# Performance work log

Hardware: AMD Instinct MI355X
Metric: run time of the kernel (lower is better)

Reference implementation:

```python
import jax, jax.numpy as jnp
import numpy as np

B, L, H, E = 8, 1024, 8, 64
S, D = 1024, 64


def fp(x):
    # power-norm with p=2: norm(x) * x^2 / norm(x^2)
    norm = jnp.sqrt(jnp.sum(x * x, axis=-1, keepdims=True))
    px = x * x  # x^p, p=2
    pnorm = jnp.sqrt(jnp.sum(px * px, axis=-1, keepdims=True))
    return norm * px / pnorm


def phi_p(x):
    return fp(jax.nn.relu(x))


def setup_inputs() -> dict:
    key = jax.random.key(0)
    kq, kk, kv = jax.random.split(key, 3)
    queries = jax.random.normal(kq, (B, L, H, E), dtype=jnp.float32)
    keys = jax.random.normal(kk, (B, S, H, E), dtype=jnp.float32)
    values = jax.random.normal(kv, (B, S, H, D), dtype=jnp.float32)
    # all-False mask: masked_fill(-inf) + fp() would NaN otherwise (see notes)
    attn_mask = jnp.zeros((B, 1, L, S), dtype=bool)
    return {"queries": queries, "keys": keys, "values": values, "attn_mask": attn_mask}


def reference(queries, keys, values, attn_mask):
    qt = phi_p(queries)              # [B,L,H,E]
    kt = phi_p(keys)                 # [B,S,H,E]
    scores = jnp.einsum('blhe,bshe->bhls', qt, kt)  # [B,H,L,S]
    scores = jnp.where(attn_mask, -jnp.inf, scores)  # mask_flag=True path
    # NB: original computes scale = 1/sqrt(E) but never applies it.
    A = jax.nn.softmax(fp(scores), axis=-1)  # dropout is identity at eval
    V = jnp.einsum('bhls,bshd->blhd', A, values)  # [B,L,H,D]
    return V
```

## Files before the change

### kernel.cpp

```cpp
#include <hip/hip_runtime.h>
#include <hip/hip_bf16.h>


#define B_ 8
#define L_ 1024
#define H_ 8
#define E_ 64
#define S_ 1024
#define D_ 64
#define BH_ 64

typedef _Float16 f16_t;
typedef _Float16 f16x8 __attribute__((ext_vector_type(8)));
typedef _Float16 f16x4v __attribute__((ext_vector_type(4)));
typedef float f32x4 __attribute__((ext_vector_type(4)));
typedef unsigned u32x4 __attribute__((ext_vector_type(4)));

#define MFMA16F(a, b, c) __builtin_amdgcn_mfma_f32_16x16x32_f16(a, b, c, 0, 0, 0)
#define GLDS16(g, l)                                                        \
  __builtin_amdgcn_global_load_lds(                                         \
      (const __attribute__((address_space(1))) void*)(g),                   \
      (__attribute__((address_space(3))) void*)(l), 16, 0, 0)

#if __has_builtin(__builtin_amdgcn_exp2f)
#define EXP2(x) __builtin_amdgcn_exp2f(x)
#else
#define EXP2(x) exp2f(x)
#endif

static __device__ __forceinline__ unsigned pkh(float a, float b) {
  return __builtin_bit_cast(unsigned, __builtin_amdgcn_cvt_pkrtz(a, b));
}

static __device__ __forceinline__ void pl32_swap(unsigned& x, unsigned& y) {
#if __has_builtin(__builtin_amdgcn_permlane32_swap)
  auto r = __builtin_amdgcn_permlane32_swap(x, y, false, false);
  x = r[0];
  y = r[1];
#else
  unsigned xs = __shfl_xor((int)x, 32, 64), ys = __shfl_xor((int)y, 32, 64);
  bool hi = (threadIdx.x & 32) != 0;
  unsigned nx = hi ? ys : x;
  unsigned ny = hi ? y : xs;
  x = nx;
  y = ny;
#endif
}

static __device__ __forceinline__ void pl16_swap(unsigned& x, unsigned& y) {
#if __has_builtin(__builtin_amdgcn_permlane16_swap)
  auto r = __builtin_amdgcn_permlane16_swap(x, y, false, false);
  x = r[0];
  y = r[1];
#else
  unsigned xs = __shfl_xor((int)x, 16, 64), ys = __shfl_xor((int)y, 16, 64);
  bool odd = (threadIdx.x & 16) != 0;
  unsigned nx = odd ? ys : x;
  unsigned ny = odd ? y : xs;
  x = nx;
  y = ny;
#endif
}

__global__ __launch_bounds__(256) void prep_kernel(
    const float* __restrict__ q, const float* __restrict__ k,
    const float* __restrict__ v, f16_t* __restrict__ qf,
    f16_t* __restrict__ kf, f16_t* __restrict__ vt) {
  __shared__ float tile[32][68];
  int bid = blockIdx.x;
  if (bid < 8192) {
    int row = bid * 16 + (threadIdx.x >> 4);
    int p = threadIdx.x & 15;
    const float* src;
    f16_t* dst;
    int r = row;
    if (r < B_ * L_ * H_) { src = q; dst = qf; }
    else { r -= B_ * L_ * H_; src = k; dst = kf; }
    int b = r >> 13;
    int l = (r >> 3) & 1023;
    int h = r & 7;
    float4 x = ((const float4*)(src + (size_t)r * 64))[p];
    float s0 = fmaxf(x.x, 0.f) * fmaxf(x.x, 0.f);
    float s1 = fmaxf(x.y, 0.f) * fmaxf(x.y, 0.f);
    float s2 = fmaxf(x.z, 0.f) * fmaxf(x.z, 0.f);
    float s3 = fmaxf(x.w, 0.f) * fmaxf(x.w, 0.f);
    float sum2 = (s0 + s1) + (s2 + s3);
    float sum4 = fmaf(s0, s0, s1 * s1) + fmaf(s2, s2, s3 * s3);
#pragma unroll
    for (int off = 1; off < 16; off <<= 1) {
      sum2 += __shfl_xor(sum2, off, 64);
      sum4 += __shfl_xor(sum4, off, 64);
    }
    float sc = (sum4 > 0.f) ? sqrtf(sum2 / sum4) : 0.f;
    f16x4v o = {(f16_t)(sc * s0), (f16_t)(sc * s1), (f16_t)(sc * s2),
                (f16_t)(sc * s3)};
    int c = p >> 1, e = (p & 1) * 4;
    int col = (((c ^ (l & 7)) << 3) | e);
    *(f16x4v*)(dst + ((size_t)(b * H_ + h) * 1024 + l) * 64 + col) = o;
  } else {
    int vb = bid - 8192;
    int bh = vb >> 5;
    int st = vb & 31;
    int b = bh >> 3, h = bh & 7;
    int t = threadIdx.x;
    int sl = t >> 3, dp = t & 7;
    const float* src =
        v + (((size_t)(b * S_ + st * 32 + sl) * H_ + h) * D_) + dp * 8;
    float4 f0 = ((const float4*)src)[0];
    float4 f1 = ((const float4*)src)[1];
    *(float4*)&tile[sl][dp * 8] = f0;
    *(float4*)&tile[sl][dp * 8 + 4] = f1;
    __syncthreads();
    int d = t >> 2, sc = t & 3;
    f16_t tmp[8];
#pragma unroll
    for (int j = 0; j < 8; ++j) tmp[j] = (f16_t)tile[sc * 8 + j][d];
    f16_t* dst = vt + (((size_t)bh * 32 + st) * 64 + d) * 32 + sc * 8;
    *(uint4*)dst = *(const uint4*)tmp;
  }
}

__global__ __launch_bounds__(256, 2) void attn_kernel(
    const f16_t* __restrict__ qf, const f16_t* __restrict__ kf,
    const f16_t* __restrict__ vt, float* __restrict__ out) {
  __shared__ __align__(16) f16_t k_t[2][2048];
  __shared__ __align__(16) f16_t v_t[2][2048];

  int bh = blockIdx.x & 63;
  int qb = blockIdx.x >> 6;
  int b = bh >> 3, h = bh & 7;
  int tid = threadIdx.x;
  int wave = tid >> 6, lane = tid & 63;
  int g = lane >> 4, n = lane & 15;

  const f16_t* qf_b = qf + ((size_t)bh * L_ + qb * 128) * 64;
  const f16_t* kf_b = kf + (size_t)bh * S_ * 64;
  const f16_t* vt_b = vt + (size_t)bh * 32 * 2048;

  int arow = wave * 32 + n;
  int qoff0 = arow * 64 + ((g ^ (n & 7)) << 3);
  int qoff1 = qoff0 + 16 * 64;
  f16x8 qa0_0 = *(const f16x8*)(qf_b + qoff0);
  f16x8 qa1_0 = *(const f16x8*)(qf_b + (qoff0 ^ 32));
  f16x8 qa0_1 = *(const f16x8*)(qf_b + qoff1);
  f16x8 qa1_1 = *(const f16x8*)(qf_b + (qoff1 ^ 32));

  int koff = n * 64 + ((g ^ (n & 7)) << 3);
  int lds_o = tid * 8;

  const f32x4 fzero = {0.f, 0.f, 0.f, 0.f};
  f32x4 acc2_0 = fzero, acc4_0 = fzero, mx_0 = fzero;
  f32x4 acc2_1 = fzero, acc4_1 = fzero, mx_1 = fzero;

  GLDS16(kf_b + lds_o, &k_t[0][lds_o]);
  for (int t = 0; t < 32; ++t) {
    __syncthreads();
    if (t < 31)
      GLDS16(kf_b + (t + 1) * 2048 + lds_o, &k_t[(t + 1) & 1][lds_o]);
    const f16_t* kt = k_t[t & 1];
    f16x8 b00 = *(const f16x8*)(kt + koff);
    f16x8 b01 = *(const f16x8*)(kt + (koff ^ 32));
    f16x8 b10 = *(const f16x8*)(kt + koff + 1024);
    f16x8 b11 = *(const f16x8*)(kt + (koff ^ 32) + 1024);
    f32x4 sc0_0 = MFMA16F(b00, qa0_0, fzero);
    sc0_0 = MFMA16F(b01, qa1_0, sc0_0);
    f32x4 sc1_0 = MFMA16F(b10, qa0_0, fzero);
    sc1_0 = MFMA16F(b11, qa1_0, sc1_0);
    f32x4 sc0_1 = MFMA16F(b00, qa0_1, fzero);
    sc0_1 = MFMA16F(b01, qa1_1, sc0_1);
    f32x4 sc1_1 = MFMA16F(b10, qa0_1, fzero);
    sc1_1 = MFMA16F(b11, qa1_1, sc1_1);
    f32x4 t0 = sc0_0 * sc0_0, t1 = sc1_0 * sc1_0;
    acc2_0 += t0 + t1;
    acc4_0 += t0 * t0;
    acc4_0 += t1 * t1;
    mx_0 = __builtin_elementwise_max(mx_0, __builtin_elementwise_max(t0, t1));
    f32x4 u0 = sc0_1 * sc0_1, u1 = sc1_1 * sc1_1;
    acc2_1 += u0 + u1;
    acc4_1 += u0 * u0;
    acc4_1 += u1 * u1;
    mx_1 = __builtin_elementwise_max(mx_1, __builtin_elementwise_max(u0, u1));
  }
  GLDS16(kf_b + lds_o, &k_t[0][lds_o]);
  GLDS16(vt_b + lds_o, &v_t[0][lds_o]);

  const float LOG2E = 1.44269504f;
  float c2_0, cm2_0, c2_1, cm2_1;
  {
    float a2 = (acc2_0[0] + acc2_0[1]) + (acc2_0[2] + acc2_0[3]);
    float a4 = (acc4_0[0] + acc4_0[1]) + (acc4_0[2] + acc4_0[3]);
    float m2 = fmaxf(fmaxf(mx_0[0], mx_0[1]), fmaxf(mx_0[2], mx_0[3]));
    a2 += __shfl_xor(a2, 16, 64);
    a4 += __shfl_xor(a4, 16, 64);
    m2 = fmaxf(m2, __shfl_xor(m2, 16, 64));
    a2 += __shfl_xor(a2, 32, 64);
    a4 += __shfl_xor(a4, 32, 64);
    m2 = fmaxf(m2, __shfl_xor(m2, 32, 64));
    c2_0 = (a4 > 0.f) ? (sqrtf(a2 / a4) * LOG2E) : 0.f;
    cm2_0 = c2_0 * m2;
  }
  {
    float a2 = (acc2_1[0] + acc2_1[1]) + (acc2_1[2] + acc2_1[3]);
    float a4 = (acc4_1[0] + acc4_1[1]) + (acc4_1[2] + acc4_1[3]);
    float m2 = fmaxf(fmaxf(mx_1[0], mx_1[1]), fmaxf(mx_1[2], mx_1[3]));
    a2 += __shfl_xor(a2, 16, 64);
    a4 += __shfl_xor(a4, 16, 64);
    m2 = fmaxf(m2, __shfl_xor(m2, 16, 64));
    a2 += __shfl_xor(a2, 32, 64);
    a4 += __shfl_xor(a4, 32, 64);
    m2 = fmaxf(m2, __shfl_xor(m2, 32, 64));
    c2_1 = (a4 > 0.f) ? (sqrtf(a2 / a4) * LOG2E) : 0.f;
    cm2_1 = c2_1 * m2;
  }

  f32x4 pv0[4], pv1[4];
#pragma unroll
  for (int dg = 0; dg < 4; ++dg) { pv0[dg] = fzero; pv1[dg] = fzero; }
  f32x4 denv0 = fzero, denv1 = fzero;

  for (int t = 0; t < 32; ++t) {
    __syncthreads();
    if (t < 31) {
      int go = (t + 1) * 2048 + lds_o;
      int bs = (t + 1) & 1;
      GLDS16(kf_b + go, &k_t[bs][lds_o]);
      GLDS16(vt_b + go, &v_t[bs][lds_o]);
    }
    const f16_t* kt = k_t[t & 1];
    const f16_t* vl = v_t[t & 1];
    f16x8 vb[4];
#pragma unroll
    for (int dg = 0; dg < 4; ++dg)
      vb[dg] = *(const f16x8*)(vl + n * 32 + dg * 512 + g * 8);
    f16x8 b00 = *(const f16x8*)(kt + koff);
    f16x8 b01 = *(const f16x8*)(kt + (koff ^ 32));
    f16x8 b10 = *(const f16x8*)(kt + koff + 1024);
    f16x8 b11 = *(const f16x8*)(kt + (koff ^ 32) + 1024);
    f32x4 sc0_0 = MFMA16F(b00, qa0_0, fzero);
    sc0_0 = MFMA16F(b01, qa1_0, sc0_0);
    f32x4 sc1_0 = MFMA16F(b10, qa0_0, fzero);
    sc1_0 = MFMA16F(b11, qa1_0, sc1_0);
    f32x4 sc0_1 = MFMA16F(b00, qa0_1, fzero);
    sc0_1 = MFMA16F(b01, qa1_1, sc0_1);
    f32x4 sc1_1 = MFMA16F(b10, qa0_1, fzero);
    sc1_1 = MFMA16F(b11, qa1_1, sc1_1);
    f32x4 e0 = sc0_0 * sc0_0 * c2_0 - cm2_0;
    f32x4 e1 = sc1_0 * sc1_0 * c2_0 - cm2_0;
    f32x4 w0, w1;
#pragma unroll
    for (int r = 0; r < 4; ++r) { w0[r] = EXP2(e0[r]); w1[r] = EXP2(e1[r]); }
    denv0 += w0 + w1;
    unsigned X0 = pkh(w0[0], w0[1]), X1 = pkh(w0[2], w0[3]);
    unsigned Y0 = pkh(w1[0], w1[1]), Y1 = pkh(w1[2], w1[3]);
    pl32_swap(X0, Y0);
    pl16_swap(X0, Y0);
    pl32_swap(X1, Y1);
    pl16_swap(X1, Y1);
    u32x4 fu0 = {X0, X1, Y0, Y1};
    f16x8 wa0 = __builtin_bit_cast(f16x8, fu0);
    f32x4 f0v = sc0_1 * sc0_1 * c2_1 - cm2_1;
    f32x4 f1v = sc1_1 * sc1_1 * c2_1 - cm2_1;
    f32x4 z0, z1;
#pragma unroll
    for (int r = 0; r < 4; ++r) { z0[r] = EXP2(f0v[r]); z1[r] = EXP2(f1v[r]); }
    denv1 += z0 + z1;
    unsigned P0 = pkh(z0[0], z0[1]), P1 = pkh(z0[2], z0[3]);
    unsigned Q0 = pkh(z1[0], z1[1]), Q1 = pkh(z1[2], z1[3]);
    pl32_swap(P0, Q0);
    pl16_swap(P0, Q0);
    pl32_swap(P1, Q1);
    pl16_swap(P1, Q1);
    u32x4 fu1 = {P0, P1, Q0, Q1};
    f16x8 wa1 = __builtin_bit_cast(f16x8, fu1);
#pragma unroll
    for (int dg = 0; dg < 4; ++dg) {
      pv0[dg] = MFMA16F(wa0, vb[dg], pv0[dg]);
      pv1[dg] = MFMA16F(wa1, vb[dg], pv1[dg]);
    }
  }

  float den0 = (denv0[0] + denv0[1]) + (denv0[2] + denv0[3]);
  den0 += __shfl_xor(den0, 16, 64);
  den0 += __shfl_xor(den0, 32, 64);
  float den1 = (denv1[0] + denv1[1]) + (denv1[2] + denv1[3]);
  den1 += __shfl_xor(den1, 16, 64);
  den1 += __shfl_xor(den1, 32, 64);
#pragma unroll
  for (int r = 0; r < 4; ++r) {
    float dr0 = __shfl(den0, g * 4 + r, 64);
    float inv0 = 1.f / dr0;
    int l0 = qb * 128 + wave * 32 + g * 4 + r;
    float* op0 = out + (((size_t)b * L_ + l0) * H_ + h) * D_;
#pragma unroll
    for (int dg = 0; dg < 4; ++dg) op0[dg * 16 + n] = pv0[dg][r] * inv0;
    float dr1 = __shfl(den1, g * 4 + r, 64);
    float inv1 = 1.f / dr1;
    int l1 = l0 + 16;
    float* op1 = out + (((size_t)b * L_ + l1) * H_ + h) * D_;
#pragma unroll
    for (int dg = 0; dg < 4; ++dg) op1[dg * 16 + n] = pv1[dg][r] * inv1;
  }
}

extern "C" void kernel_launch(void* const* d_in, const int* in_sizes, int n_in,
                              void* d_out, int out_size, void* d_ws, size_t ws_size,
                              hipStream_t stream) {
  const float* q = (const float*)d_in[0];
  const float* k = (const float*)d_in[1];
  const float* v = (const float*)d_in[2];
  float* out = (float*)d_out;

  const size_t NE = (size_t)B_ * L_ * H_ * E_;
  f16_t* qf = (f16_t*)d_ws;
  f16_t* kf = qf + NE;
  f16_t* vt = kf + NE;

  prep_kernel<<<8192 + 2048, 256, 0, stream>>>(q, k, v, qf, kf, vt);
  attn_kernel<<<BH_ * (L_ / 128), 256, 0, stream>>>(qf, kf, vt, out);
}
```

Baseline: 155.0 us.

## Split key sequence across two wave groups per block and merge partials via LDS

Doubles the block to 512 threads, with each half processing half of the key/value sequence for both the statistics pass and the PV pass, then merging norm statistics and partial outputs through shared memory. This halves the serial loop length per wave and raises the number of active waves given only 512 blocks. Also XOR-swizzles the transposed V layout to reduce LDS bank conflicts on V reads. Costs extra LDS, extra barriers and a merge step.

```diff
diff --git a/kernel.cpp b/kernel.cpp
--- a/kernel.cpp
+++ b/kernel.cpp
@@ -115,29 +115,32 @@
     f16_t tmp[8];
 #pragma unroll
     for (int j = 0; j < 8; ++j) tmp[j] = (f16_t)tile[sc * 8 + j][d];
-    f16_t* dst = vt + (((size_t)bh * 32 + st) * 64 + d) * 32 + sc * 8;
+    f16_t* dst =
+        vt + (((size_t)bh * 32 + st) * 64 + d) * 32 + (sc ^ ((d >> 1) & 3)) * 8;
     *(uint4*)dst = *(const uint4*)tmp;
   }
 }
 
-__global__ __launch_bounds__(256, 2) void attn_kernel(
+__global__ __launch_bounds__(512, 4) void attn_kernel(
     const f16_t* __restrict__ qf, const f16_t* __restrict__ kf,
     const f16_t* __restrict__ vt, float* __restrict__ out) {
-  __shared__ __align__(16) f16_t k_t[2][2048];
-  __shared__ __align__(16) f16_t v_t[2][2048];
+  __shared__ __align__(16) f16_t k_t[2][2][2048];
+  __shared__ __align__(16) f16_t v_t[2][2][2048];
+  __shared__ __align__(16) float mrg[4][64][34];
 
   int bh = blockIdx.x & 63;
   int qb = blockIdx.x >> 6;
   int b = bh >> 3, h = bh & 7;
   int tid = threadIdx.x;
   int wave = tid >> 6, lane = tid & 63;
+  int wv = wave & 3, sh = wave >> 2;
   int g = lane >> 4, n = lane & 15;
 
   const f16_t* qf_b = qf + ((size_t)bh * L_ + qb * 128) * 64;
-  const f16_t* kf_b = kf + (size_t)bh * S_ * 64;
-  const f16_t* vt_b = vt + (size_t)bh * 32 * 2048;
-
-  int arow = wave * 32 + n;
+  const f16_t* kf_b = kf + (size_t)bh * S_ * 64 + (size_t)sh * 16 * 2048;
+  const f16_t* vt_b = vt + (size_t)bh * 32 * 2048 + (size_t)sh * 16 * 2048;
+
+  int arow = wv * 32 + n;
   int qoff0 = arow * 64 + ((g ^ (n & 7)) << 3);
   int qoff1 = qoff0 + 16 * 64;
   f16x8 qa0_0 = *(const f16x8*)(qf_b + qoff0);
@@ -146,18 +149,19 @@
   f16x8 qa1_1 = *(const f16x8*)(qf_b + (qoff1 ^ 32));
 
   int koff = n * 64 + ((g ^ (n & 7)) << 3);
-  int lds_o = tid * 8;
+  int voff = n * 32 + ((g ^ ((n >> 1) & 3)) << 3);
+  int so = (tid & 255) * 8;
 
   const f32x4 fzero = {0.f, 0.f, 0.f, 0.f};
   f32x4 acc2_0 = fzero, acc4_0 = fzero, mx_0 = fzero;
   f32x4 acc2_1 = fzero, acc4_1 = fzero, mx_1 = fzero;
 
-  GLDS16(kf_b + lds_o, &k_t[0][lds_o]);
-  for (int t = 0; t < 32; ++t) {
+  GLDS16(kf_b + so, &k_t[sh][0][so]);
+  for (int t = 0; t < 16; ++t) {
     __syncthreads();
-    if (t < 31)
-      GLDS16(kf_b + (t + 1) * 2048 + lds_o, &k_t[(t + 1) & 1][lds_o]);
-    const f16_t* kt = k_t[t & 1];
+    if (t < 15)
+      GLDS16(kf_b + (t + 1) * 2048 + so, &k_t[sh][(t + 1) & 1][so]);
+    const f16_t* kt = k_t[sh][t & 1];
     f16x8 b00 = *(const f16x8*)(kt + koff);
     f16x8 b01 = *(const f16x8*)(kt + (koff ^ 32));
     f16x8 b10 = *(const f16x8*)(kt + koff + 1024);
@@ -181,57 +185,64 @@
     acc4_1 += u1 * u1;
     mx_1 = __builtin_elementwise_max(mx_1, __builtin_elementwise_max(u0, u1));
   }
-  GLDS16(kf_b + lds_o, &k_t[0][lds_o]);
-  GLDS16(vt_b + lds_o, &v_t[0][lds_o]);
-
+  GLDS16(kf_b + so, &k_t[sh][0][so]);
+  GLDS16(vt_b + so, &v_t[sh][0][so]);
+
+  float a2_0 = (acc2_0[0] + acc2_0[1]) + (acc2_0[2] + acc2_0[3]);
+  float a4_0 = (acc4_0[0] + acc4_0[1]) + (acc4_0[2] + acc4_0[3]);
+  float m2_0 = fmaxf(fmaxf(mx_0[0], mx_0[1]), fmaxf(mx_0[2], mx_0[3]));
+  float a2_1 = (acc2_1[0] + acc2_1[1]) + (acc2_1[2] + acc2_1[3]);
+  float a4_1 = (acc4_1[0] + acc4_1[1]) + (acc4_1[2] + acc4_1[3]);
+  float m2_1 = fmaxf(fmaxf(mx_1[0], mx_1[1]), fmaxf(mx_1[2], mx_1[3]));
+  a2_0 += __shfl_xor(a2_0, 16, 64);
+  a4_0 += __shfl_xor(a4_0, 16, 64);
+  m2_0 = fmaxf(m2_0, __shfl_xor(m2_0, 16, 64));
+  a2_1 += __shfl_xor(a2_1, 16, 64);
+  a4_1 += __shfl_xor(a4_1, 16, 64);
+  m2_1 = fmaxf(m2_1, __shfl_xor(m2_1, 16, 64));
+  a2_0 += __shfl_xor(a2_0, 32, 64);
+  a4_0 += __shfl_xor(a4_0, 32, 64);
+  m2_0 = fmaxf(m2_0, __shfl_xor(m2_0, 32, 64));
+  a2_1 += __shfl_xor(a2_1, 32, 64);
+  a4_1 += __shfl_xor(a4_1, 32, 64);
+  m2_1 = fmaxf(m2_1, __shfl_xor(m2_1, 32, 64));
+
+  {
+    float* sm = &mrg[0][0][0] + ((size_t)(wave * 64 + lane)) * 6;
+    sm[0] = a2_0; sm[1] = a4_0; sm[2] = m2_0;
+    sm[3] = a2_1; sm[4] = a4_1; sm[5] = m2_1;
+  }
+  __syncthreads();
+  {
+    const float* sp = &mrg[0][0][0] + ((size_t)((wave ^ 4) * 64 + lane)) * 6;
+    a2_0 += sp[0]; a4_0 += sp[1]; m2_0 = fmaxf(m2_0, sp[2]);
+    a2_1 += sp[3]; a4_1 += sp[4]; m2_1 = fmaxf(m2_1, sp[5]);
+  }
   const float LOG2E = 1.44269504f;
-  float c2_0, cm2_0, c2_1, cm2_1;
-  {
-    float a2 = (acc2_0[0] + acc2_0[1]) + (acc2_0[2] + acc2_0[3]);
-    float a4 = (acc4_0[0] + acc4_0[1]) + (acc4_0[2] + acc4_0[3]);
-    float m2 = fmaxf(fmaxf(mx_0[0], mx_0[1]), fmaxf(mx_0[2], mx_0[3]));
-    a2 += __shfl_xor(a2, 16, 64);
-    a4 += __shfl_xor(a4, 16, 64);
-    m2 = fmaxf(m2, __shfl_xor(m2, 16, 64));
-    a2 += __shfl_xor(a2, 32, 64);
-    a4 += __shfl_xor(a4, 32, 64);
-    m2 = fmaxf(m2, __shfl_xor(m2, 32, 64));
-    c2_0 = (a4 > 0.f) ? (sqrtf(a2 / a4) * LOG2E) : 0.f;
-    cm2_0 = c2_0 * m2;
-  }
-  {
-    float a2 = (acc2_1[0] + acc2_1[1]) + (acc2_1[2] + acc2_1[3]);
-    float a4 = (acc4_1[0] + acc4_1[1]) + (acc4_1[2] + acc4_1[3]);
-    float m2 = fmaxf(fmaxf(mx_1[0], mx_1[1]), fmaxf(mx_1[2], mx_1[3]));
-    a2 += __shfl_xor(a2, 16, 64);
-    a4 += __shfl_xor(a4, 16, 64);
-    m2 = fmaxf(m2, __shfl_xor(m2, 16, 64));
-    a2 += __shfl_xor(a2, 32, 64);
-    a4 += __shfl_xor(a4, 32, 64);
-    m2 = fmaxf(m2, __shfl_xor(m2, 32, 64));
-    c2_1 = (a4 > 0.f) ? (sqrtf(a2 / a4) * LOG2E) : 0.f;
-    cm2_1 = c2_1 * m2;
-  }
+  float c2_0 = (a4_0 > 0.f) ? (sqrtf(a2_0 / a4_0) * LOG2E) : 0.f;
+  float cm2_0 = c2_0 * m2_0;
+  float c2_1 = (a4_1 > 0.f) ? (sqrtf(a2_1 / a4_1) * LOG2E) : 0.f;
+  float cm2_1 = c2_1 * m2_1;
 
   f32x4 pv0[4], pv1[4];
 #pragma unroll
   for (int dg = 0; dg < 4; ++dg) { pv0[dg] = fzero; pv1[dg] = fzero; }
   f32x4 denv0 = fzero, denv1 = fzero;
 
-  for (int t = 0; t < 32; ++t) {
+  for (int t = 0; t < 16; ++t) {
     __syncthreads();
-    if (t < 31) {
-      int go = (t + 1) * 2048 + lds_o;
+    if (t < 15) {
+      int go = (t + 1) * 2048 + so;
       int bs = (t + 1) & 1;
-      GLDS16(kf_b + go, &k_t[bs][lds_o]);
-      GLDS16(vt_b + go, &v_t[bs][lds_o]);
+      GLDS16(kf_b + go, &k_t[sh][bs][so]);
+      GLDS16(vt_b + go, &v_t[sh][bs][so]);
     }
-    const f16_t* kt = k_t[t & 1];
-    const f16_t* vl = v_t[t & 1];
+    const f16_t* kt = k_t[sh][t & 1];
+    const f16_t* vl = v_t[sh][t & 1];
     f16x8 vb[4];
 #pragma unroll
     for (int dg = 0; dg < 4; ++dg)
-      vb[dg] = *(const f16x8*)(vl + n * 32 + dg * 512 + g * 8);
+      vb[dg] = *(const f16x8*)(vl + voff + dg * 512);
     f16x8 b00 = *(const f16x8*)(kt + koff);
     f16x8 b01 = *(const f16x8*)(kt + (koff ^ 32));
     f16x8 b10 = *(const f16x8*)(kt + koff + 1024);
@@ -285,20 +296,47 @@
   float den1 = (denv1[0] + denv1[1]) + (denv1[2] + denv1[3]);
   den1 += __shfl_xor(den1, 16, 64);
   den1 += __shfl_xor(den1, 32, 64);
-#pragma unroll
-  for (int r = 0; r < 4; ++r) {
-    float dr0 = __shfl(den0, g * 4 + r, 64);
-    float inv0 = 1.f / dr0;
-    int l0 = qb * 128 + wave * 32 + g * 4 + r;
-    float* op0 = out + (((size_t)b * L_ + l0) * H_ + h) * D_;
-#pragma unroll
-    for (int dg = 0; dg < 4; ++dg) op0[dg * 16 + n] = pv0[dg][r] * inv0;
-    float dr1 = __shfl(den1, g * 4 + r, 64);
-    float inv1 = 1.f / dr1;
-    int l1 = l0 + 16;
-    float* op1 = out + (((size_t)b * L_ + l1) * H_ + h) * D_;
-#pragma unroll
-    for (int dg = 0; dg < 4; ++dg) op1[dg * 16 + n] = pv1[dg][r] * inv1;
+
+  __syncthreads();
+  if (sh == 1) {
+    float* mp = &mrg[wv][lane][0];
+#pragma unroll
+    for (int dg = 0; dg < 4; ++dg)
+#pragma unroll
+      for (int r = 0; r < 4; ++r) {
+        mp[dg * 4 + r] = pv0[dg][r];
+        mp[16 + dg * 4 + r] = pv1[dg][r];
+      }
+    mp[32] = den0;
+    mp[33] = den1;
+  }
+  __syncthreads();
+  if (sh == 0) {
+    const float* mp = &mrg[wv][lane][0];
+#pragma unroll
+    for (int dg = 0; dg < 4; ++dg)
+#pragma unroll
+      for (int r = 0; r < 4; ++r) {
+        pv0[dg][r] += mp[dg * 4 + r];
+        pv1[dg][r] += mp[16 + dg * 4 + r];
+      }
+    den0 += mp[32];
+    den1 += mp[33];
+#pragma unroll
+    for (int r = 0; r < 4; ++r) {
+      float dr0 = __shfl(den0, g * 4 + r, 64);
+      float inv0 = 1.f / dr0;
+      int l0 = qb * 128 + wv * 32 + g * 4 + r;
+      float* op0 = out + (((size_t)b * L_ + l0) * H_ + h) * D_;
+#pragma unroll
+      for (int dg = 0; dg < 4; ++dg) op0[dg * 16 + n] = pv0[dg][r] * inv0;
+      float dr1 = __shfl(den1, g * 4 + r, 64);
+      float inv1 = 1.f / dr1;
+      int l1 = l0 + 16;
+      float* op1 = out + (((size_t)b * L_ + l1) * H_ + h) * D_;
+#pragma unroll
+      for (int dg = 0; dg < 4; ++dg) op1[dg * 16 + n] = pv1[dg][r] * inv1;
+    }
   }
 }
 
@@ -316,5 +354,5 @@
   f16_t* vt = kf + NE;
 
   prep_kernel<<<8192 + 2048, 256, 0, stream>>>(q, k, v, qf, kf, vt);
-  attn_kernel<<<BH_ * (L_ / 128), 256, 0, stream>>>(qf, kf, vt, out);
-}
+  attn_kernel<<<BH_ * (L_ / 128), 512, 0, stream>>>(qf, kf, vt, out);
+}
```

After: 147.3 us. 1.05x faster.
